# Kernel tuning notes

Measured on AMD Instinct MI355X. Metric: run time of the kernel, lower is better.

The kernel has to match this reference:

```python
import jax, jax.numpy as jnp
import numpy as np

N, MAX_SIZE, SPATIAL = 50000, 32, 27
CH_IN, CH_OUT = 128, 128


def setup_inputs() -> dict:
    key = jax.random.key(0)
    k1, k2, k3, k4 = jax.random.split(key, 4)
    feat_in = jax.random.normal(k1, (N, CH_IN), dtype=jnp.float32)
    select_mat = jax.random.uniform(k2, (N, MAX_SIZE, SPATIAL), dtype=jnp.float32)
    # kaiming-uniform-ish init for weight of shape [SPATIAL, CH_OUT*CH_IN]
    fan_in = CH_OUT * CH_IN
    bound = np.sqrt(6.0 / fan_in)
    weight = jax.random.uniform(k3, (SPATIAL, CH_OUT * CH_IN), dtype=jnp.float32,
                                minval=-bound, maxval=bound)
    neighbor_idx = jax.random.randint(k4, (N, MAX_SIZE), 0, N, dtype=jnp.int64)
    return {"feat_in": feat_in, "select_mat": select_mat,
            "weight": weight, "neighbor_idx": neighbor_idx}


def reference(feat_in, select_mat, weight, neighbor_idx):
    # feat_in: [N, I]; select_mat: [N, M, S]; weight: [S, O*I]; neighbor_idx: [N, M]
    ch_in = feat_in.shape[1]
    spatial = weight.shape[0]
    ch_out = weight.shape[1] // ch_in
    w = weight.reshape(spatial, ch_out, ch_in)          # [S, O, I]
    patch_feat = feat_in[neighbor_idx]                  # irregular gather -> [N, M, I]
    # Original math: out[n,o] = sum_m sum_s sel[n,m,s] * W[s,o,i] * pf[n,m,i]
    # Contract neighbor dim first to avoid the [N, M, O, I] intermediate.
    t = jnp.einsum('nms,nmi->nsi', select_mat, patch_feat)   # [N, S, I]
    feat_out = jnp.einsum('nsi,soi->no', t, w)               # [N, O]
    return feat_out[:, :, None]                              # [N, O, 1]
```

## Files before the change

kernel.cpp:

```cpp
#include <hip/hip_runtime.h>


#define N_CHI 128
#define N_SP  27
#define N_M   32
#define KDIM  (N_SP * N_CHI)
#define SEL_STRIDE (N_M * N_SP)

typedef short s16x8 __attribute__((ext_vector_type(8)));
typedef s16x8 __attribute__((may_alias)) s16x8_a;
typedef unsigned short u16x8 __attribute__((ext_vector_type(8)));
typedef u16x8 __attribute__((may_alias)) u16x8_a;
typedef unsigned int u32x2 __attribute__((ext_vector_type(2)));
typedef u32x2 __attribute__((may_alias)) u32x2_a;
typedef float f32x4 __attribute__((ext_vector_type(4)));
typedef f32x4 __attribute__((may_alias)) f32x4_a;
typedef float f32x16 __attribute__((ext_vector_type(16)));

typedef __attribute__((address_space(3))) unsigned int as3_u32;
typedef __attribute__((address_space(1))) const unsigned int as1_u32;

static __device__ __forceinline__ unsigned short f2bf(float f) {
  unsigned int u = __float_as_uint(f);
  u += 0x7FFFu + ((u >> 16) & 1u);
  return (unsigned short)(u >> 16);
}

__global__ __launch_bounds__(128) void wconv_kernel(const float* __restrict__ w,
                                                    unsigned short* __restrict__ Wt) {
  const int s = blockIdx.x;
  const int o = blockIdx.y;
  const int i = threadIdx.x;
  Wt[((size_t)o * N_SP + s) * N_CHI + i] = f2bf(w[((size_t)s * 128 + o) * N_CHI + i]);
}

__global__ __launch_bounds__(256) void featbf_kernel(const float* __restrict__ feat,
                                                     unsigned short* __restrict__ fb,
                                                     int total4) {
  const int i = blockIdx.x * 256 + threadIdx.x;
  if (i >= total4) return;
  f32x4 v = *(const f32x4_a*)&feat[(size_t)i * 4];
  u32x2 o;
  o[0] = (unsigned int)f2bf(v[0]) | ((unsigned int)f2bf(v[1]) << 16);
  o[1] = (unsigned int)f2bf(v[2]) | ((unsigned int)f2bf(v[3]) << 16);
  *(u32x2_a*)&fb[(size_t)i * 4] = o;
}

__global__ __launch_bounds__(256, 5) void phase1_kernel(
    const unsigned short* __restrict__ featbf, const float* __restrict__ sel,
    const int* __restrict__ nidx, unsigned short* __restrict__ T,
    int nbase, int nend) {
  __shared__ __align__(16) unsigned short tbuf[4][N_SP * 128];
  const int wave = threadIdx.x >> 6;
  const int lane = threadIdx.x & 63;
  const int n = nbase + (int)blockIdx.x * 4 + wave;
  if (n >= nend) return;
  unsigned short* tb = tbuf[wave];
  const int q = lane >> 5;
  const int col = lane & 31;
  const bool sv = (col < N_SP);

  const float* selp = sel + (size_t)n * SEL_STRIDE;
  s16x8 bf0, bf1;
#pragma unroll
  for (int j = 0; j < 8; ++j) {
    const int m0 = q * 8 + j;
    float v0 = sv ? selp[m0 * N_SP + col] : 0.0f;
    float v1 = sv ? selp[(16 + m0) * N_SP + col] : 0.0f;
    bf0[j] = (short)f2bf(v0);
    bf1[j] = (short)f2bf(v1);
  }

  const int* ip = nidx + (size_t)n * N_M;
  int offe[16];
#pragma unroll
  for (int ks = 0; ks < 2; ++ks)
#pragma unroll
    for (int j = 0; j < 8; ++j)
      offe[ks * 8 + j] = ip[ks * 16 + q * 8 + j] * N_CHI;

#pragma unroll
  for (int ti = 0; ti < 4; ++ti) {
    const int icol = ti * 32 + col;
    s16x8 af0, af1;
#pragma unroll
    for (int j = 0; j < 8; ++j) {
      af0[j] = (short)featbf[offe[j] + icol];
      af1[j] = (short)featbf[offe[8 + j] + icol];
    }
    f32x16 acc = {0.f, 0.f, 0.f, 0.f, 0.f, 0.f, 0.f, 0.f,
                  0.f, 0.f, 0.f, 0.f, 0.f, 0.f, 0.f, 0.f};
    acc = __builtin_amdgcn_mfma_f32_32x32x16_bf16(af0, bf0, acc, 0, 0, 0);
    acc = __builtin_amdgcn_mfma_f32_32x32x16_bf16(af1, bf1, acc, 0, 0, 0);
    if (sv) {
#pragma unroll
      for (int g = 0; g < 4; ++g) {
        const int sub = ti * 8 + g * 2 + q;
        const int phys = col * 128 + (((sub ^ ((col & 7) << 2))) << 2);
        u32x2 pk;
        pk[0] = (unsigned int)f2bf(acc[4 * g + 0]) | ((unsigned int)f2bf(acc[4 * g + 1]) << 16);
        pk[1] = (unsigned int)f2bf(acc[4 * g + 2]) | ((unsigned int)f2bf(acc[4 * g + 3]) << 16);
        *(u32x2_a*)&tb[phys] = pk;
      }
    }
  }

  unsigned short* Tn = T + (size_t)(n - nbase) * KDIM;
#pragma unroll
  for (int it = 0; it < 7; ++it) {
    const int P = it * 64 + lane;
    if (P < 432) {
      const int c = P >> 4;
      const int sub = (P << 1) & 31;
      const int phys = c * 128 + (((sub ^ ((c & 7) << 2))) << 2);
      *(u16x8_a*)&Tn[(size_t)P * 8] = *(const u16x8_a*)&tb[phys];
    }
  }
}

__global__ __launch_bounds__(256) void phase2_kernel(
    const unsigned short* __restrict__ T, const unsigned short* __restrict__ Wt,
    float* __restrict__ out, int nbase, int N) {
  __shared__ __align__(16) unsigned short Alds[3][128 * 64];
  __shared__ __align__(16) unsigned short Blds[3][128 * 64];
  const int tid = threadIdx.x;
  const int lane = tid & 63;
  const int wbase = tid & ~63;
  const int wave = tid >> 6;
  const int wm = wave & 1, wn = wave >> 1;
  const int quad = lane >> 4, l16 = lane & 15;
  const size_t rowbase = (size_t)blockIdx.x * 128;

  f32x4 acc[4][4];
#pragma unroll
  for (int a = 0; a < 4; ++a)
#pragma unroll
    for (int b = 0; b < 4; ++b) acc[a][b] = (f32x4){0.f, 0.f, 0.f, 0.f};

  const unsigned short* aga[4];
  const unsigned short* bga[4];
#pragma unroll
  for (int it = 0; it < 4; ++it) {
    const int slot = it * 256 + tid;
    const int r = slot >> 3, bp = slot & 7;
    aga[it] = T + (rowbase + r) * KDIM + ((bp ^ (r & 7)) << 3);
    bga[it] = Wt + (size_t)r * KDIM + ((bp ^ (r & 7)) << 3);
  }

  auto stage = [&](int buf, int k0) {
#pragma unroll
    for (int it = 0; it < 4; ++it) {
      __builtin_amdgcn_global_load_lds(
          (as1_u32*)(const void*)(aga[it] + k0),
          (as3_u32*)(void*)&Alds[buf][(it * 256 + wbase) * 8], 16, 0, 0);
      __builtin_amdgcn_global_load_lds(
          (as1_u32*)(const void*)(bga[it] + k0),
          (as3_u32*)(void*)&Blds[buf][(it * 256 + wbase) * 8], 16, 0, 0);
    }
  };

  auto compute = [&](int cur) {
#pragma unroll
    for (int ks = 0; ks < 2; ++ks) {
      const int bg = ks * 4 + quad;
      s16x8 af[4], bfr[4];
#pragma unroll
      for (int mt = 0; mt < 4; ++mt) {
        const int m = wm * 64 + mt * 16 + l16;
        af[mt] = *(const s16x8_a*)&Alds[cur][m * 64 + ((bg ^ (m & 7)) << 3)];
      }
#pragma unroll
      for (int nt = 0; nt < 4; ++nt) {
        const int o = wn * 64 + nt * 16 + l16;
        bfr[nt] = *(const s16x8_a*)&Blds[cur][o * 64 + ((bg ^ (o & 7)) << 3)];
      }
#pragma unroll
      for (int mt = 0; mt < 4; ++mt)
#pragma unroll
        for (int nt = 0; nt < 4; ++nt)
          acc[mt][nt] = __builtin_amdgcn_mfma_f32_16x16x32_bf16(af[mt], bfr[nt],
                                                                acc[mt][nt], 0, 0, 0);
    }
  };

  const int NKT = KDIM / 64;
  stage(0, 0);
  stage(1, 64);

  for (int kt = 0; kt < NKT; ++kt) {
    if (kt < NKT - 1) asm volatile("s_waitcnt vmcnt(8)" ::: "memory");
    else              asm volatile("s_waitcnt vmcnt(0)" ::: "memory");
    asm volatile("s_waitcnt lgkmcnt(0)" ::: "memory");
    __builtin_amdgcn_s_barrier();
    asm volatile("" ::: "memory");
    if (kt + 2 < NKT) stage((kt + 2) % 3, (kt + 2) * 64);
    compute(kt % 3);
  }

#pragma unroll
  for (int mt = 0; mt < 4; ++mt) {
    const int growb = nbase + (int)rowbase + wm * 64 + mt * 16 + quad * 4;
#pragma unroll
    for (int r = 0; r < 4; ++r) {
      const int grow = growb + r;
      if (grow < N) {
#pragma unroll
        for (int nt = 0; nt < 4; ++nt) {
          const int o = wn * 64 + nt * 16 + l16;
          out[(size_t)grow * 128 + o] = acc[mt][nt][r];
        }
      }
    }
  }
}

extern "C" void kernel_launch(void* const* d_in, const int* in_sizes, int n_in,
                              void* d_out, int out_size, void* d_ws, size_t ws_size,
                              hipStream_t stream) {
  const float* feat = (const float*)d_in[0];
  const float* sel  = (const float*)d_in[1];
  const float* wgt  = (const float*)d_in[2];
  const int*   nidx = (const int*)d_in[3];
  float* out = (float*)d_out;
  const int N = in_sizes[0] / N_CHI;

  unsigned short* Wt = (unsigned short*)d_ws;
  const size_t WT_ELEMS = (size_t)128 * KDIM;
  unsigned short* FB = Wt + WT_ELEMS;
  const size_t FB_ELEMS = (size_t)N * N_CHI;
  unsigned short* T = FB + FB_ELEMS;

  wconv_kernel<<<dim3(N_SP, 128), 128, 0, stream>>>(wgt, Wt);
  const int total4 = (int)(FB_ELEMS / 4);
  featbf_kernel<<<dim3((unsigned)((total4 + 255) / 256)), 256, 0, stream>>>(
      feat, FB, total4);

  const size_t used = (WT_ELEMS + FB_ELEMS) * 2;
  const size_t bytes_for_T = (ws_size > used) ? (ws_size - used) : 0;
  long cap_rows = (long)(bytes_for_T / ((size_t)KDIM * 2));
  long NC = (cap_rows / 128) * 128;
  const long Nfull = (((long)N + 127) / 128) * 128;
  if (NC > Nfull) NC = Nfull;
  if (NC <= 0) return;

  for (long nb = 0; nb < N; nb += NC) {
    long rows = (long)N - nb;
    if (rows > NC) rows = NC;
    const long rows128 = ((rows + 127) / 128) * 128;
    phase1_kernel<<<dim3((unsigned)((rows + 3) / 4)), 256, 0, stream>>>(
        FB, sel, nidx, T, (int)nb, (int)(nb + rows));
    phase2_kernel<<<dim3((unsigned)(rows128 / 128)), 256, 0, stream>>>(
        T, Wt, out, (int)nb, N);
  }
}
```

Baseline: 546.9 us.

## Shrink phase2 GEMM tile to 64 rows and drop LDS triple buffering for occupancy

The phase2 GEMM now uses a 64-row M tile instead of 128, with a single LDS buffer and __syncthreads around each K step instead of a three-deep async prefetch pipeline. Launch bounds request four blocks per CU, and the grid doubles. The aim is more resident waves to hide memory latency through occupancy instead of software pipelining. In exchange it loses load/compute overlap within a block, re-reads the weight tile twice as often, and adds two barriers per K step.

```diff
diff --git a/kernel.cpp b/kernel.cpp
--- a/kernel.cpp
+++ b/kernel.cpp
@@ -118,88 +118,81 @@
   }
 }
 
-__global__ __launch_bounds__(256) void phase2_kernel(
+__global__ __launch_bounds__(256, 4) void phase2_kernel(
     const unsigned short* __restrict__ T, const unsigned short* __restrict__ Wt,
     float* __restrict__ out, int nbase, int N) {
-  __shared__ __align__(16) unsigned short Alds[3][128 * 64];
-  __shared__ __align__(16) unsigned short Blds[3][128 * 64];
+  __shared__ __align__(16) unsigned short Alds[64 * 64];
+  __shared__ __align__(16) unsigned short Blds[128 * 64];
   const int tid = threadIdx.x;
   const int lane = tid & 63;
   const int wbase = tid & ~63;
   const int wave = tid >> 6;
   const int wm = wave & 1, wn = wave >> 1;
   const int quad = lane >> 4, l16 = lane & 15;
-  const size_t rowbase = (size_t)blockIdx.x * 128;
-
-  f32x4 acc[4][4];
-#pragma unroll
-  for (int a = 0; a < 4; ++a)
+  const size_t rowbase = (size_t)blockIdx.x * 64;
+
+  f32x4 acc[2][4];
+#pragma unroll
+  for (int a = 0; a < 2; ++a)
 #pragma unroll
     for (int b = 0; b < 4; ++b) acc[a][b] = (f32x4){0.f, 0.f, 0.f, 0.f};
 
-  const unsigned short* aga[4];
+  const unsigned short* aga[2];
   const unsigned short* bga[4];
+#pragma unroll
+  for (int it = 0; it < 2; ++it) {
+    const int slot = it * 256 + tid;
+    const int r = slot >> 3, bp = slot & 7;
+    aga[it] = T + (rowbase + r) * KDIM + ((bp ^ (r & 7)) << 3);
+  }
 #pragma unroll
   for (int it = 0; it < 4; ++it) {
     const int slot = it * 256 + tid;
     const int r = slot >> 3, bp = slot & 7;
-    aga[it] = T + (rowbase + r) * KDIM + ((bp ^ (r & 7)) << 3);
     bga[it] = Wt + (size_t)r * KDIM + ((bp ^ (r & 7)) << 3);
   }
 
-  auto stage = [&](int buf, int k0) {
-#pragma unroll
-    for (int it = 0; it < 4; ++it) {
+  const int NKT = KDIM / 64;
+  for (int kt = 0; kt < NKT; ++kt) {
+    const int k0 = kt * 64;
+#pragma unroll
+    for (int it = 0; it < 2; ++it)
       __builtin_amdgcn_global_load_lds(
           (as1_u32*)(const void*)(aga[it] + k0),
-          (as3_u32*)(void*)&Alds[buf][(it * 256 + wbase) * 8], 16, 0, 0);
+          (as3_u32*)(void*)&Alds[(it * 256 + wbase) * 8], 16, 0, 0);
+#pragma unroll
+    for (int it = 0; it < 4; ++it)
       __builtin_amdgcn_global_load_lds(
           (as1_u32*)(const void*)(bga[it] + k0),
-          (as3_u32*)(void*)&Blds[buf][(it * 256 + wbase) * 8], 16, 0, 0);
-    }
-  };
-
-  auto compute = [&](int cur) {
+          (as3_u32*)(void*)&Blds[(it * 256 + wbase) * 8], 16, 0, 0);
+    __syncthreads();
 #pragma unroll
     for (int ks = 0; ks < 2; ++ks) {
       const int bg = ks * 4 + quad;
-      s16x8 af[4], bfr[4];
-#pragma unroll
-      for (int mt = 0; mt < 4; ++mt) {
-        const int m = wm * 64 + mt * 16 + l16;
-        af[mt] = *(const s16x8_a*)&Alds[cur][m * 64 + ((bg ^ (m & 7)) << 3)];
+      s16x8 af[2], bfr[4];
+#pragma unroll
+      for (int mt = 0; mt < 2; ++mt) {
+        const int m = wm * 32 + mt * 16 + l16;
+        af[mt] = *(const s16x8_a*)&Alds[m * 64 + ((bg ^ (m & 7)) << 3)];
       }
 #pragma unroll
       for (int nt = 0; nt < 4; ++nt) {
         const int o = wn * 64 + nt * 16 + l16;
-        bfr[nt] = *(const s16x8_a*)&Blds[cur][o * 64 + ((bg ^ (o & 7)) << 3)];
-      }
-#pragma unroll
-      for (int mt = 0; mt < 4; ++mt)
+        bfr[nt] = *(const s16x8_a*)&Blds[o * 64 + ((bg ^ (o & 7)) << 3)];
+      }
+#pragma unroll
+      for (int mt = 0; mt < 2; ++mt)
 #pragma unroll
         for (int nt = 0; nt < 4; ++nt)
           acc[mt][nt] = __builtin_amdgcn_mfma_f32_16x16x32_bf16(af[mt], bfr[nt],
                                                                 acc[mt][nt], 0, 0, 0);
     }
-  };
-
-  const int NKT = KDIM / 64;
-  stage(0, 0);
-  stage(1, 64);
-
-  for (int kt = 0; kt < NKT; ++kt) {
-    if (kt < NKT - 1) asm volatile("s_waitcnt vmcnt(8)" ::: "memory");
-    else              asm volatile("s_waitcnt vmcnt(0)" ::: "memory");
-    asm volatile("s_waitcnt lgkmcnt(0)" ::: "memory");
-    __builtin_amdgcn_s_barrier();
-    asm volatile("" ::: "memory");
-    if (kt + 2 < NKT) stage((kt + 2) % 3, (kt + 2) * 64);
-    compute(kt % 3);
-  }
-
-#pragma unroll
-  for (int mt = 0; mt < 4; ++mt) {
-    const int growb = nbase + (int)rowbase + wm * 64 + mt * 16 + quad * 4;
+    __syncthreads();
+  }
+
+#pragma unroll
+  for (int mt = 0; mt < 2; ++mt) {
+    const int growb = nbase + (int)rowbase + wm * 32 + mt * 16 + quad * 4;
 #pragma unroll
     for (int r = 0; r < 4; ++r) {
       const int grow = growb + r;
@@ -246,10 +239,10 @@
   for (long nb = 0; nb < N; nb += NC) {
     long rows = (long)N - nb;
     if (rows > NC) rows = NC;
-    const long rows128 = ((rows + 127) / 128) * 128;
+    const long rows64 = ((rows + 63) / 64) * 64;
     phase1_kernel<<<dim3((unsigned)((rows + 3) / 4)), 256, 0, stream>>>(
         FB, sel, nidx, T, (int)nb, (int)(nb + rows));
-    phase2_kernel<<<dim3((unsigned)(rows128 / 128)), 256, 0, stream>>>(
+    phase2_kernel<<<dim3((unsigned)(rows64 / 64)), 256, 0, stream>>>(
         T, Wt, out, (int)nb, N);
   }
 }
```

Measured after the change: 498.3 us. 1.1x faster.
